# Optimization experiments

Hardware: AMD Instinct MI355X
Metric: run time of the kernel (lower is better)

Reference implementation:

```python
import jax, jax.numpy as jnp
import numpy as np


def _bilinear_gather(corr, x, y):
    # corr: [N, H2, W2]; x, y: [N, K, K] pixel coords; zero padding outside,
    # matching F.grid_sample(mode='bilinear', padding_mode='zeros', align_corners=True).
    N, H2, W2 = corr.shape
    corr_flat = corr.reshape(N, H2 * W2)
    x0 = jnp.floor(x)
    y0 = jnp.floor(y)
    wx1 = x - x0
    wy1 = y - y0

    def gather(xi, yi):
        valid = (xi >= 0) & (xi <= W2 - 1) & (yi >= 0) & (yi <= H2 - 1)
        xc = jnp.clip(xi, 0, W2 - 1).astype(jnp.int32)
        yc = jnp.clip(yi, 0, H2 - 1).astype(jnp.int32)
        idx = (yc * W2 + xc).reshape(N, -1)
        vals = jnp.take_along_axis(corr_flat, idx, axis=1).reshape(xi.shape)
        return jnp.where(valid, vals, jnp.zeros((), corr.dtype))

    return (gather(x0, y0) * (1 - wx1) * (1 - wy1)
            + gather(x0 + 1, y0) * wx1 * (1 - wy1)
            + gather(x0, y0 + 1) * (1 - wx1) * wy1
            + gather(x0 + 1, y0 + 1) * wx1 * wy1)


def setup_inputs() -> dict:
    key = jax.random.key(0)
    k1, k2, k3 = jax.random.split(key, 3)
    B, D, H, W = 2, 256, 64, 64
    fmap1 = jax.random.normal(k1, (B, D, H, W), dtype=jnp.float32)
    fmap2 = jax.random.normal(k2, (B, D, H, W), dtype=jnp.float32)
    # coords in pixel space [0, W-1]
    coords = jax.random.uniform(k3, (B, 2, H, W), dtype=jnp.float32) * (W - 1)
    return {"fmap1": fmap1, "fmap2": fmap2, "coords": coords, "radius": 4}


def reference(fmap1, fmap2, coords, radius):
    B, D, H, W = fmap1.shape
    # all-pairs correlation: [B, H*W, H*W], scaled by 1/sqrt(D)
    f1 = fmap1.reshape(B, D, H * W)
    f2 = fmap2.reshape(B, D, H * W)
    corr = jnp.einsum('bdn,bdm->bnm', f1, f2) / jnp.sqrt(jnp.asarray(D, jnp.float32))
    corr = corr.reshape(B * H * W, H, W)

    r = radius
    K = 2 * r + 1
    d = jnp.linspace(-r, r, K, dtype=jnp.float32)
    dyg, dxg = jnp.meshgrid(d, d, indexing='ij')
    delta = jnp.stack([dyg, dxg], axis=-1)  # [K, K, 2] (matches torch.meshgrid(dy, dx))

    centroid = coords.transpose(0, 2, 3, 1).reshape(B * H * W, 1, 1, 2)
    coords_lvl = centroid + delta[None]  # [N, K, K, 2]
    # RAFT bilinear_sampler: channel 0 is x, channel 1 is y
    x = coords_lvl[..., 0]
    y = coords_lvl[..., 1]

    out = _bilinear_gather(corr, x, y)  # [N, K, K]
    out = out.reshape(B, H, W, K * K).transpose(0, 3, 1, 2)
    return out.astype(jnp.float32)
```

## Files before the change

### kernel.cpp

```cpp
#include <hip/hip_runtime.h>

#define HWC 4096
#define WC 64
#define HC 64
#define DC 256
#define BC 2
#define KKC 81

typedef _Float16 h2 __attribute__((ext_vector_type(2)));
typedef _Float16 h8 __attribute__((ext_vector_type(8)));

static __device__ inline float dot8(h8 v, h8 a, float s) {
#if __has_builtin(__builtin_amdgcn_fdot2)
    s = __builtin_amdgcn_fdot2((h2){v[0], v[1]}, (h2){a[0], a[1]}, s, false);
    s = __builtin_amdgcn_fdot2((h2){v[2], v[3]}, (h2){a[2], a[3]}, s, false);
    s = __builtin_amdgcn_fdot2((h2){v[4], v[5]}, (h2){a[4], a[5]}, s, false);
    s = __builtin_amdgcn_fdot2((h2){v[6], v[7]}, (h2){a[6], a[7]}, s, false);
#else
#pragma unroll
    for (int k = 0; k < 8; ++k) s += (float)v[k] * (float)a[k];
#endif
    return s;
}

#define DPP_ADD(x, ctrl) \
    ((x) + __int_as_float(__builtin_amdgcn_update_dpp(0, __float_as_int(x), (ctrl), 0xF, 0xF, true)))

__global__ __launch_bounds__(256) void transpose_h_k(const float* __restrict__ in0,
                                                     _Float16* __restrict__ out0) {
    __shared__ float tile[64][33];
    const int b = blockIdx.z;
    const float* in = in0 + (size_t)b * DC * HWC;
    _Float16* out = out0 + (size_t)b * HWC * DC;
    const int m0 = blockIdx.x * 32, d0 = blockIdx.y * 64;
    const int tid = threadIdx.x;

    const int tx = tid & 31, ty = tid >> 5;
#pragma unroll
    for (int k = 0; k < 8; ++k)
        tile[ty + k * 8][tx] = in[(size_t)(d0 + ty + k * 8) * HWC + m0 + tx];
    __syncthreads();

    const int dx = tid & 7, my = tid >> 3;
    h8 v;
#pragma unroll
    for (int e = 0; e < 8; ++e) v[e] = (_Float16)tile[dx * 8 + e][my];
    *(h8*)(out + (size_t)(m0 + my) * DC + d0 + dx * 8) = v;
}

__global__ __launch_bounds__(256) void corr_k(const float* __restrict__ f1,
                                              const _Float16* __restrict__ f2t,
                                              const float* __restrict__ coords,
                                              float* __restrict__ out) {
    __shared__ float Cs[112];
    __shared__ float f1s[DC];

    const int bid = blockIdx.x;
    const int xcd = bid & 7;
    const int b = xcd >> 2;
    const int hw = ((bid >> 3) << 2) + (xcd & 3);

    const int tid = threadIdx.x;
    const int g = tid >> 4;
    const int l = tid & 15;

    f1s[tid] = f1[((size_t)b * DC + tid) * HWC + hw];

    const float x = coords[((size_t)b * 2 + 0) * HWC + hw];
    const float y = coords[((size_t)b * 2 + 1) * HWC + hw];
    const float x0f = floorf(x), y0f = floorf(y);
    const float wx = x - x0f, wy = y - y0f;
    const int ix0 = (int)x0f, iy0 = (int)y0f;
    __syncthreads();

    const float* fp = f1s + l * 16;
    h8 a0, a1;
#pragma unroll
    for (int e = 0; e < 8; ++e) { a0[e] = (_Float16)fp[e]; a1[e] = (_Float16)fp[8 + e]; }

    const h8* f2b = (const h8*)f2t + (size_t)b * HWC * 32;

#pragma unroll
    for (int it = 0; it < 7; ++it) {
        const int t = it * 16 + g;
        const int yi = t / 10, xi = t - yi * 10;
        const int gy = iy0 - 4 + yi, gx = ix0 - 4 + xi;
        const int gyc = min(max(gy, 0), HC - 1);
        const int gxc = min(max(gx, 0), WC - 1);
        const bool valid = ((unsigned)gy < (unsigned)HC) &
                           ((unsigned)gx < (unsigned)WC) & (t < 100);
        const h8* vp = f2b + (size_t)(gyc * WC + gxc) * 32 + l * 2;
        const h8 v0 = vp[0], v1 = vp[1];
        float s = dot8(v0, a0, 0.f);
        s = dot8(v1, a1, s);
        s = valid ? s : 0.f;
        s = DPP_ADD(s, 0xB1);
        s = DPP_ADD(s, 0x4E);
        s = DPP_ADD(s, 0x124);
        s = DPP_ADD(s, 0x128);
        if (l == 0) Cs[t] = s * 0.0625f;
    }
    __syncthreads();

    if (tid < KKC) {
        const int i = tid / 9, j = tid % 9;
        const float w00 = (1.f - wx) * (1.f - wy);
        const float w01 = wx * (1.f - wy);
        const float w10 = (1.f - wx) * wy;
        const float w11 = wx * wy;
        const float r = w00 * Cs[j * 10 + i]       + w01 * Cs[j * 10 + i + 1] +
                        w10 * Cs[(j + 1) * 10 + i] + w11 * Cs[(j + 1) * 10 + i + 1];
        out[((size_t)(b * KKC + tid)) * HWC + hw] = r;
    }
}

extern "C" void kernel_launch(void* const* d_in, const int* in_sizes, int n_in,
                              void* d_out, int out_size, void* d_ws, size_t ws_size,
                              hipStream_t stream) {
    const float* fmap1 = (const float*)d_in[0];
    const float* fmap2 = (const float*)d_in[1];
    const float* coords = (const float*)d_in[2];
    float* out = (float*)d_out;

    _Float16* f2t = (_Float16*)d_ws;

    transpose_h_k<<<dim3(HWC / 32, DC / 64, BC), dim3(256), 0, stream>>>(fmap2, f2t);
    corr_k<<<dim3(BC * HWC), dim3(256), 0, stream>>>(fmap1, f2t, coords, out);
}
```

Baseline: 96.70 us.

## Pre-transpose fmap1 to fp16 and batch all neighbor loads before dot products

```diff
diff --git a/kernel.cpp b/kernel.cpp
--- a/kernel.cpp
+++ b/kernel.cpp
@@ -26,15 +26,20 @@
 #define DPP_ADD(x, ctrl) \
     ((x) + __int_as_float(__builtin_amdgcn_update_dpp(0, __float_as_int(x), (ctrl), 0xF, 0xF, true)))
 
-__global__ __launch_bounds__(256) void transpose_h_k(const float* __restrict__ in0,
-                                                     _Float16* __restrict__ out0) {
+__global__ __launch_bounds__(256) void transpose_h_k(const float* __restrict__ f1,
+                                                     const float* __restrict__ f2,
+                                                     _Float16* __restrict__ o1,
+                                                     _Float16* __restrict__ o2) {
     __shared__ float tile[64][33];
-    const int b = blockIdx.z;
-    const float* in = in0 + (size_t)b * DC * HWC;
-    _Float16* out = out0 + (size_t)b * HWC * DC;
+    const int z = blockIdx.z;
+    const int b = z & 1;
+    const float* in = (z >> 1) ? f2 : f1;
+    _Float16* out = (z >> 1) ? o2 : o1;
+    in += (size_t)b * DC * HWC;
+    out += (size_t)b * HWC * DC;
+
     const int m0 = blockIdx.x * 32, d0 = blockIdx.y * 64;
     const int tid = threadIdx.x;
-
     const int tx = tid & 31, ty = tid >> 5;
 #pragma unroll
     for (int k = 0; k < 8; ++k)
@@ -48,12 +53,11 @@
     *(h8*)(out + (size_t)(m0 + my) * DC + d0 + dx * 8) = v;
 }
 
-__global__ __launch_bounds__(256) void corr_k(const float* __restrict__ f1,
+__global__ __launch_bounds__(256) void corr_k(const _Float16* __restrict__ f1t,
                                               const _Float16* __restrict__ f2t,
                                               const float* __restrict__ coords,
                                               float* __restrict__ out) {
     __shared__ float Cs[112];
-    __shared__ float f1s[DC];
 
     const int bid = blockIdx.x;
     const int xcd = bid & 7;
@@ -64,41 +68,44 @@
     const int g = tid >> 4;
     const int l = tid & 15;
 
-    f1s[tid] = f1[((size_t)b * DC + tid) * HWC + hw];
-
     const float x = coords[((size_t)b * 2 + 0) * HWC + hw];
     const float y = coords[((size_t)b * 2 + 1) * HWC + hw];
     const float x0f = floorf(x), y0f = floorf(y);
     const float wx = x - x0f, wy = y - y0f;
     const int ix0 = (int)x0f, iy0 = (int)y0f;
-    __syncthreads();
 
-    const float* fp = f1s + l * 16;
-    h8 a0, a1;
+    const h8* ap = (const h8*)f1t + ((size_t)(b * HWC + hw)) * 32 + l * 2;
+    const h8 a0 = ap[0], a1 = ap[1];
+    const h8* f2b = (const h8*)f2t + (size_t)b * HWC * 32;
+
+    h8 v0[7], v1[7];
+    float vm[7];
 #pragma unroll
-    for (int e = 0; e < 8; ++e) { a0[e] = (_Float16)fp[e]; a1[e] = (_Float16)fp[8 + e]; }
-
-    const h8* f2b = (const h8*)f2t + (size_t)b * HWC * 32;
+    for (int it = 0; it < 7; ++it) {
+        int t = it * 16 + g;
+        t = t > 99 ? 99 : t;
+        const int yi = t / 10, xi = t - yi * 10;
+        const int gy = iy0 - 4 + yi, gx = ix0 - 4 + xi;
+        const bool valid = ((unsigned)gy < (unsigned)HC) & ((unsigned)gx < (unsigned)WC);
+        const int gyc = min(max(gy, 0), HC - 1);
+        const int gxc = min(max(gx, 0), WC - 1);
+        const h8* vp = f2b + (size_t)(gyc * WC + gxc) * 32 + l * 2;
+        v0[it] = vp[0];
+        v1[it] = vp[1];
+        vm[it] = valid ? 0.0625f : 0.f;
+    }
 
 #pragma unroll
     for (int it = 0; it < 7; ++it) {
-        const int t = it * 16 + g;
-        const int yi = t / 10, xi = t - yi * 10;
-        const int gy = iy0 - 4 + yi, gx = ix0 - 4 + xi;
-        const int gyc = min(max(gy, 0), HC - 1);
-        const int gxc = min(max(gx, 0), WC - 1);
-        const bool valid = ((unsigned)gy < (unsigned)HC) &
-                           ((unsigned)gx < (unsigned)WC) & (t < 100);
-        const h8* vp = f2b + (size_t)(gyc * WC + gxc) * 32 + l * 2;
-        const h8 v0 = vp[0], v1 = vp[1];
-        float s = dot8(v0, a0, 0.f);
-        s = dot8(v1, a1, s);
-        s = valid ? s : 0.f;
+        float s = dot8(v0[it], a0, 0.f);
+        s = dot8(v1[it], a1, s);
+        s *= vm[it];
         s = DPP_ADD(s, 0xB1);
         s = DPP_ADD(s, 0x4E);
         s = DPP_ADD(s, 0x124);
         s = DPP_ADD(s, 0x128);
-        if (l == 0) Cs[t] = s * 0.0625f;
+        const int t = it * 16 + g;
+        if (l == 0 && t < 100) Cs[t] = s;
     }
     __syncthreads();
 
@@ -122,8 +129,10 @@
     const float* coords = (const float*)d_in[2];
     float* out = (float*)d_out;
 
-    _Float16* f2t = (_Float16*)d_ws;
+    const size_t perH = (size_t)BC * HWC * DC;
+    _Float16* f1t = (_Float16*)d_ws;
+    _Float16* f2t = f1t + perH;
 
-    transpose_h_k<<<dim3(HWC / 32, DC / 64, BC), dim3(256), 0, stream>>>(fmap2, f2t);
-    corr_k<<<dim3(BC * HWC), dim3(256), 0, stream>>>(fmap1, f2t, coords, out);
+    transpose_h_k<<<dim3(HWC / 32, DC / 64, 4), dim3(256), 0, stream>>>(fmap1, fmap2, f1t, f2t);
+    corr_k<<<dim3(BC * HWC), dim3(256), 0, stream>>>(f1t, f2t, coords, out);
 }
```

After: 92.51 us. 1.05x faster.
